# Kernel optimization log

Measured on AMD Instinct MI355X. Metric: run time of the kernel, lower is better.

Reference implementation:

```python
import jax, jax.numpy as jnp
import numpy as np
import math

B, T, D = 2, 2048, 4096
H, HD = 32, 128  # n_head, head_dim; H*HD == D
THETA = 10000.0


def _rope_tables(T, hd, theta):
    # standard RoPE: freqs_i = theta^(-2i/hd), angle[t,i] = t * freqs_i
    inv = 1.0 / (theta ** (np.arange(0, hd, 2, dtype=np.float32) / hd))  # [hd/2]
    ang = np.arange(T, dtype=np.float32)[:, None] * inv[None, :]          # [T, hd/2]
    return jnp.asarray(np.cos(ang)), jnp.asarray(np.sin(ang))


def setup_inputs() -> dict:
    key = jax.random.key(0)
    ks = jax.random.split(key, 5)
    scale = 1.0 / math.sqrt(D)
    x = jax.random.normal(ks[0], (B, T, D), dtype=jnp.float32)
    Wq = jax.random.normal(ks[1], (D, H * HD), dtype=jnp.float32) * scale
    Wk = jax.random.normal(ks[2], (D, H * HD), dtype=jnp.float32) * scale
    Wv = jax.random.normal(ks[3], (D, H * HD), dtype=jnp.float32) * scale
    Wo = jax.random.normal(ks[4], (D, D), dtype=jnp.float32) * scale
    fc, fs = _rope_tables(T, HD, THETA)
    return {"x": x, "freqs_cos": fc, "freqs_sin": fs,
            "Wq": Wq, "Wk": Wk, "Wv": Wv, "Wo": Wo}


def _apply_rope(t, cos, sin):
    # t: [B, T, H, HD]; complex rotation on interleaved (even, odd) pairs
    tp = t.reshape(*t.shape[:-1], HD // 2, 2)
    xr, xi = tp[..., 0], tp[..., 1]
    c = cos[None, :, None, :]  # [1, T, 1, HD/2]
    s = sin[None, :, None, :]
    out_r = xr * c - xi * s
    out_i = xr * s + xi * c
    return jnp.stack([out_r, out_i], axis=-1).reshape(t.shape)


def reference(x, freqs_cos, freqs_sin, Wq, Wk, Wv, Wo):
    Bc, Tc, _ = x.shape
    q = (x @ Wq).reshape(Bc, Tc, H, HD)
    k = (x @ Wk).reshape(Bc, Tc, H, HD)
    v = (x @ Wv).reshape(Bc, Tc, H, HD)
    q = _apply_rope(q, freqs_cos, freqs_sin)
    k = _apply_rope(k, freqs_cos, freqs_sin)
    scale = 1.0 / math.sqrt(HD)
    scores = jnp.einsum('bqhd,bkhd->bhqk', q, k) * scale  # [B,H,T,T]
    causal = jnp.tril(jnp.ones((Tc, Tc), dtype=bool))
    scores = jnp.where(causal[None, None], scores, -jnp.inf)
    attn = jax.nn.softmax(scores, axis=-1)
    y = jnp.einsum('bhqk,bkhd->bqhd', attn, v).reshape(Bc, Tc, H * HD)
    return y @ Wo
```

## Files before the change

kernel.cpp:

```cpp
#include <hip/hip_runtime.h>

typedef unsigned short ushort_t;
typedef unsigned int uint32;

typedef float f32x4 __attribute__((ext_vector_type(4)));
typedef __bf16 bf16x8 __attribute__((ext_vector_type(8)));
typedef unsigned short us8 __attribute__((ext_vector_type(8)));
typedef unsigned short us4 __attribute__((ext_vector_type(4)));

#define TSEQ 2048
#define DMODEL 4096

__device__ __forceinline__ ushort_t f2bf(float f) {
  uint32 u = __builtin_bit_cast(uint32, f);
  u += 0x7FFFu + ((u >> 16) & 1u);
  return (ushort_t)(u >> 16);
}
__device__ __forceinline__ float bf2f(ushort_t u) {
  return __builtin_bit_cast(float, ((uint32)u) << 16);
}

__device__ __forceinline__ void gload_lds16(const void* g, void* l) {
  auto gp = (const __attribute__((address_space(1))) void*)g;
  auto lp = (__attribute__((address_space(3))) void*)l;
  __builtin_amdgcn_global_load_lds(gp, lp, 16, 0, 0);
}

__global__ __launch_bounds__(256) void k_cast_bf16(const float* __restrict__ in,
                                                   ushort_t* __restrict__ out, int n4) {
  int g = blockIdx.x * 256 + threadIdx.x;
  if (g >= n4) return;
  float4 v = *(const float4*)(in + (size_t)g * 4);
  us4 o; o[0] = f2bf(v.x); o[1] = f2bf(v.y); o[2] = f2bf(v.z); o[3] = f2bf(v.w);
  *(us4*)(out + (size_t)g * 4) = o;
}

__global__ __launch_bounds__(256) void k_transpose_cast(const float* __restrict__ W,
                                                        ushort_t* __restrict__ WT) {
  __shared__ __align__(16) ushort_t ts[64 * 72];
  const int tid = threadIdx.x;
  const int n0 = blockIdx.x * 64, k0 = blockIdx.y * 64;
  #pragma unroll
  for (int it = 0; it < 4; ++it) {
    int e = it * 256 + tid;
    int r = e >> 4, c4 = e & 15;
    float4 v = *(const float4*)(W + (size_t)(k0 + r) * DMODEL + n0 + c4 * 4);
    us4 o; o[0] = f2bf(v.x); o[1] = f2bf(v.y); o[2] = f2bf(v.z); o[3] = f2bf(v.w);
    *(us4*)&ts[r * 72 + c4 * 4] = o;
  }
  __syncthreads();
  #pragma unroll
  for (int it = 0; it < 4; ++it) {
    int e = it * 256 + tid;
    int r2 = e >> 4, c4 = e & 15;
    us4 o;
    #pragma unroll
    for (int j = 0; j < 4; ++j) o[j] = ts[(c4 * 4 + j) * 72 + r2];
    *(us4*)(WT + (size_t)(n0 + r2) * DMODEL + k0 + c4 * 4) = o;
  }
}

template <bool OUT_BF16>
__global__ __launch_bounds__(512, 2)
void k_gemm256(const ushort_t* __restrict__ A, const ushort_t* __restrict__ Bt,
               void* __restrict__ Cv, int M, int N, int K) {
  __shared__ __align__(16) ushort_t As[2][256 * 64];
  __shared__ __align__(16) ushort_t Bs[2][256 * 64];
  const int tid = threadIdx.x;
  const int w = tid >> 6, l = tid & 63;
  const int wr = w >> 2, wc = w & 3;
  const int lg = l >> 4, lc = l & 15;

  const int nwg = gridDim.x;
  const int cpx = nwg >> 3;
  const int wg = (blockIdx.x & 7) * cpx + (blockIdx.x >> 3);
  const int nbn = N >> 8;
  const int bm = wg / nbn, bn = wg % nbn;

  const int rowoff = l >> 3;
  const int swzck  = (l & 7) ^ rowoff;
  const ushort_t* Ab = A + (size_t)(bm * 256) * K;
  const ushort_t* Bb = Bt + (size_t)(bn * 256) * K;
  const ushort_t* gA[4]; const ushort_t* gB[4];
  int ldsOff[4];
  #pragma unroll
  for (int j = 0; j < 4; ++j) {
    int r0 = (w * 4 + j) * 8;
    gA[j] = Ab + (size_t)(r0 + rowoff) * K + swzck * 8;
    gB[j] = Bb + (size_t)(r0 + rowoff) * K + swzck * 8;
    ldsOff[j] = r0 * 64;
  }

  int offA[8][2], offB[4][2];
  #pragma unroll
  for (int m = 0; m < 8; ++m)
    #pragma unroll
    for (int kk = 0; kk < 2; ++kk)
      offA[m][kk] = (wr * 128 + m * 16 + lc) * 64 + (((kk * 4 + lg) ^ (lc & 7)) * 8);
  #pragma unroll
  for (int n = 0; n < 4; ++n)
    #pragma unroll
    for (int kk = 0; kk < 2; ++kk)
      offB[n][kk] = (wc * 64 + n * 16 + lc) * 64 + (((kk * 4 + lg) ^ (lc & 7)) * 8);

  f32x4 acc[8][4];
  #pragma unroll
  for (int m = 0; m < 8; ++m)
    #pragma unroll
    for (int n = 0; n < 4; ++n) acc[m][n] = (f32x4){0.f, 0.f, 0.f, 0.f};

  #pragma unroll
  for (int j = 0; j < 4; ++j) {
    gload_lds16(gA[j], &As[0][ldsOff[j]]);
    gload_lds16(gB[j], &Bs[0][ldsOff[j]]);
  }
  #pragma unroll
  for (int j = 0; j < 4; ++j) {
    gload_lds16(gA[j] + 64, &As[1][ldsOff[j]]);
    gload_lds16(gB[j] + 64, &Bs[1][ldsOff[j]]);
  }
  asm volatile("s_waitcnt vmcnt(8)" ::: "memory");
  __builtin_amdgcn_s_barrier();
  __builtin_amdgcn_sched_barrier(0);

  const int NT = K >> 6;
  for (int t = 0; t < NT; ++t) {
    const int cur = t & 1;
    const ushort_t* Ac = As[cur];
    const ushort_t* Bc = Bs[cur];
    bf16x8 af[4][2], bf0[2][2], bf1[2][2];

    #pragma unroll
    for (int i = 0; i < 4; ++i)
      #pragma unroll
      for (int kk = 0; kk < 2; ++kk)
        af[i][kk] = *(const bf16x8*)&Ac[offA[i][kk]];
    #pragma unroll
    for (int j2 = 0; j2 < 2; ++j2)
      #pragma unroll
      for (int kk = 0; kk < 2; ++kk)
        bf0[j2][kk] = *(const bf16x8*)&Bc[offB[j2][kk]];
    asm volatile("" ::: "memory");
    __builtin_amdgcn_s_barrier();
    __builtin_amdgcn_s_setprio(1);
    #pragma unroll
    for (int i = 0; i < 4; ++i)
      #pragma unroll
      for (int j2 = 0; j2 < 2; ++j2)
        #pragma unroll
        for (int kk = 0; kk < 2; ++kk)
          acc[i][j2] = __builtin_amdgcn_mfma_f32_16x16x32_bf16(af[i][kk], bf0[j2][kk], acc[i][j2], 0, 0, 0);
    __builtin_amdgcn_s_setprio(0);
    __builtin_amdgcn_s_barrier();
    asm volatile("" ::: "memory");

    #pragma unroll
    for (int j2 = 0; j2 < 2; ++j2)
      #pragma unroll
      for (int kk = 0; kk < 2; ++kk)
        bf1[j2][kk] = *(const bf16x8*)&Bc[offB[2 + j2][kk]];
    asm volatile("" ::: "memory");
    __builtin_amdgcn_s_barrier();
    __builtin_amdgcn_s_setprio(1);
    #pragma unroll
    for (int i = 0; i < 4; ++i)
      #pragma unroll
      for (int j2 = 0; j2 < 2; ++j2)
        #pragma unroll
        for (int kk = 0; kk < 2; ++kk)
          acc[i][2 + j2] = __builtin_amdgcn_mfma_f32_16x16x32_bf16(af[i][kk], bf1[j2][kk], acc[i][2 + j2], 0, 0, 0);
    __builtin_amdgcn_s_setprio(0);
    __builtin_amdgcn_s_barrier();
    asm volatile("" ::: "memory");

    #pragma unroll
    for (int i = 0; i < 4; ++i)
      #pragma unroll
      for (int kk = 0; kk < 2; ++kk)
        af[i][kk] = *(const bf16x8*)&Ac[offA[4 + i][kk]];
    asm volatile("" ::: "memory");
    __builtin_amdgcn_s_barrier();
    __builtin_amdgcn_s_setprio(1);
    #pragma unroll
    for (int i = 0; i < 4; ++i)
      #pragma unroll
      for (int j2 = 0; j2 < 2; ++j2)
        #pragma unroll
        for (int kk = 0; kk < 2; ++kk)
          acc[4 + i][j2] = __builtin_amdgcn_mfma_f32_16x16x32_bf16(af[i][kk], bf0[j2][kk], acc[4 + i][j2], 0, 0, 0);
    __builtin_amdgcn_s_setprio(0);
    __builtin_amdgcn_s_barrier();
    asm volatile("" ::: "memory");

    if (t + 2 < NT) {
      const int k0 = (t + 2) << 6;
      #pragma unroll
      for (int j = 0; j < 4; ++j) {
        gload_lds16(gA[j] + k0, &As[cur][ldsOff[j]]);
        gload_lds16(gB[j] + k0, &Bs[cur][ldsOff[j]]);
      }
    }
    asm volatile("" ::: "memory");
    __builtin_amdgcn_s_barrier();
    __builtin_amdgcn_s_setprio(1);
    #pragma unroll
    for (int i = 0; i < 4; ++i)
      #pragma unroll
      for (int j2 = 0; j2 < 2; ++j2)
        #pragma unroll
        for (int kk = 0; kk < 2; ++kk)
          acc[4 + i][2 + j2] = __builtin_amdgcn_mfma_f32_16x16x32_bf16(af[i][kk], bf1[j2][kk], acc[4 + i][2 + j2], 0, 0, 0);
    __builtin_amdgcn_s_setprio(0);

    if (t + 2 < NT) {
      asm volatile("s_waitcnt vmcnt(8)" ::: "memory");
    } else if (t + 1 < NT) {
      asm volatile("s_waitcnt vmcnt(0)" ::: "memory");
    }
    if (t + 1 < NT) {
      __builtin_amdgcn_s_barrier();
      __builtin_amdgcn_sched_barrier(0);
    }
  }

  #pragma unroll
  for (int m = 0; m < 8; ++m) {
    int row0 = bm * 256 + wr * 128 + m * 16 + lg * 4;
    #pragma unroll
    for (int n = 0; n < 4; ++n) {
      int col = bn * 256 + wc * 64 + n * 16 + lc;
      #pragma unroll
      for (int r = 0; r < 4; ++r) {
        float v = acc[m][n][r];
        if (OUT_BF16) ((ushort_t*)Cv)[(size_t)(row0 + r) * N + col] = f2bf(v);
        else          ((float*)Cv)[(size_t)(row0 + r) * N + col] = v;
      }
    }
  }
}

__global__ __launch_bounds__(256) void k_rope(ushort_t* __restrict__ q, ushort_t* __restrict__ k,
                                              const float* __restrict__ fc,
                                              const float* __restrict__ fs) {
  int g = blockIdx.x * 256 + threadIdx.x;
  size_t base = (size_t)g * 8;
  int row = (int)(base >> 12);
  int col = (int)(base & 4095);
  int t = row & (TSEQ - 1);
  int i0 = (col & 127) >> 1;
  float4 c = *(const float4*)(fc + t * 64 + i0);
  float4 s = *(const float4*)(fs + t * 64 + i0);
  ushort_t* bufs[2] = {q, k};
  #pragma unroll
  for (int bi = 0; bi < 2; ++bi) {
    us8 v = *(const us8*)(bufs[bi] + base);
    us8 o;
    float xr, xi;
    xr = bf2f(v[0]); xi = bf2f(v[1]);
    o[0] = f2bf(xr * c.x - xi * s.x); o[1] = f2bf(xr * s.x + xi * c.x);
    xr = bf2f(v[2]); xi = bf2f(v[3]);
    o[2] = f2bf(xr * c.y - xi * s.y); o[3] = f2bf(xr * s.y + xi * c.y);
    xr = bf2f(v[4]); xi = bf2f(v[5]);
    o[4] = f2bf(xr * c.z - xi * s.z); o[5] = f2bf(xr * s.z + xi * c.z);
    xr = bf2f(v[6]); xi = bf2f(v[7]);
    o[6] = f2bf(xr * c.w - xi * s.w); o[7] = f2bf(xr * s.w + xi * c.w);
    *(us8*)(bufs[bi] + base) = o;
  }
}

__global__ __launch_bounds__(512, 2)
void k_attn(const ushort_t* __restrict__ Q, const ushort_t* __restrict__ Kb,
            const ushort_t* __restrict__ Vt, ushort_t* __restrict__ Y) {
  __shared__ __align__(16) ushort_t Ks[2][64 * 128];
  __shared__ __align__(16) ushort_t Vs[2][128 * 64];
  __shared__ __align__(16) ushort_t Ps[8][16 * 64];
  const int id = blockIdx.x;
  const int xcd = id & 7, slot = id >> 3;
  const int bx = slot & 7, gHi = slot >> 3;
  const int g = gHi * 8 + xcd;
  const int h = g & 31, b = g >> 5;
  const int tid = threadIdx.x;
  const int w = tid >> 6, l = tid & 63;
  const int lg = l >> 4, lc = l & 15;
  const float scale = 0.08838834764831845f;
  const float THR = 8.0f;

  auto stageKV = [&](int kv0, int buf) {
    #pragma unroll
    for (int i = 0; i < 2; ++i) {
      int seg = w * 2 + i;
      {
        int row = seg * 4 + (l >> 4);
        int csrc = (l & 15) ^ (row & 7);
        gload_lds16(Kb + (size_t)(b * TSEQ + kv0 + row) * DMODEL + h * 128 + csrc * 8,
                    &Ks[buf][seg * 512]);
      }
      {
        int row = seg * 8 + (l >> 3);
        int csrc = (l & 7) ^ (l >> 3);
        gload_lds16(Vt + (size_t)(h * 128 + row) * DMODEL + b * TSEQ + kv0 + csrc * 8,
                    &Vs[buf][seg * 512]);
      }
    }
  };

  for (int qi = 0; qi < 2; ++qi) {
    const int qt = qi ? (15 - bx) : bx;
    const int q0 = qt * 128;
    const int wrow0 = q0 + w * 16;

    bf16x8 qf[4];
    {
      const ushort_t* qp = Q + (size_t)(b * TSEQ + wrow0 + lc) * DMODEL + h * 128;
      #pragma unroll
      for (int ks = 0; ks < 4; ++ks) qf[ks] = *(const bf16x8*)(qp + ks * 32 + lg * 8);
    }

    float m_r[4], lp[4];
    #pragma unroll
    for (int r = 0; r < 4; ++r) { m_r[r] = -1e30f; lp[r] = 0.f; }
    f32x4 o[8];
    #pragma unroll
    for (int t = 0; t < 8; ++t) o[t] = (f32x4){0.f, 0.f, 0.f, 0.f};

    const int nkv = (qt + 1) * 2;
    stageKV(0, 0);
    for (int kt = 0; kt < nkv; ++kt) {
      const int cur = kt & 1;
      const int kv0 = kt * 64;
      if (kt + 1 < nkv) {
        stageKV((kt + 1) * 64, cur ^ 1);
        asm volatile("s_waitcnt vmcnt(4)" ::: "memory");
      } else {
        asm volatile("s_waitcnt vmcnt(0)" ::: "memory");
      }
      __builtin_amdgcn_s_barrier();

      if (kv0 <= wrow0 + 15) {
        f32x4 s[4];
        __builtin_amdgcn_s_setprio(1);
        #pragma unroll
        for (int n = 0; n < 4; ++n) {
          s[n] = (f32x4){0.f, 0.f, 0.f, 0.f};
          #pragma unroll
          for (int ks = 0; ks < 4; ++ks) {
            int row = n * 16 + lc;
            bf16x8 kf = *(const bf16x8*)&Ks[cur][row * 128 + ((ks * 32 + lg * 8) ^ ((row & 7) * 8))];
            s[n] = __builtin_amdgcn_mfma_f32_16x16x32_bf16(qf[ks], kf, s[n], 0, 0, 0);
          }
        }
        __builtin_amdgcn_s_setprio(0);

        float sv[4][4];
        if (kv0 + 63 > wrow0) {
          #pragma unroll
          for (int n = 0; n < 4; ++n)
            #pragma unroll
            for (int r = 0; r < 4; ++r) {
              float x = s[n][r] * scale;
              int kvg = kv0 + n * 16 + lc;
              int qg = wrow0 + lg * 4 + r;
              sv[n][r] = (kvg > qg) ? -1e30f : x;
            }
        } else {
          #pragma unroll
          for (int n = 0; n < 4; ++n)
            #pragma unroll
            for (int r = 0; r < 4; ++r) sv[n][r] = s[n][r] * scale;
        }

        float pmax[4];
        #pragma unroll
        for (int r = 0; r < 4; ++r)
          pmax[r] = fmaxf(fmaxf(sv[0][r], sv[1][r]), fmaxf(sv[2][r], sv[3][r]));
        bool ok = (pmax[0] <= m_r[0] + THR) && (pmax[1] <= m_r[1] + THR) &&
                  (pmax[2] <= m_r[2] + THR) && (pmax[3] <= m_r[3] + THR);
        if (!__all(ok)) {
          #pragma unroll
          for (int r = 0; r < 4; ++r) {
            float mx = pmax[r];
            #pragma unroll
            for (int off = 1; off < 16; off <<= 1) mx = fmaxf(mx, __shfl_xor(mx, off, 16));
            float mn = fmaxf(m_r[r], mx);
            float al = __expf(m_r[r] - mn);
            m_r[r] = mn;
            lp[r] *= al;
            #pragma unroll
            for (int t = 0; t < 8; ++t) o[t][r] *= al;
          }
        }

        #pragma unroll
        for (int n = 0; n < 4; ++n)
          #pragma unroll
          for (int r = 0; r < 4; ++r) {
            float p = __expf(sv[n][r] - m_r[r]);
            lp[r] += p;
            int row = lg * 4 + r, col = n * 16 + lc;
            Ps[w][row * 64 + (col ^ (lg * 16))] = f2bf(p);
          }

        __builtin_amdgcn_s_setprio(1);
        #pragma unroll
        for (int kvs = 0; kvs < 2; ++kvs) {
          bf16x8 pa = *(const bf16x8*)&Ps[w][lc * 64 + ((kvs * 32 + lg * 8) ^ ((lc >> 2) * 16))];
          #pragma unroll
          for (int t = 0; t < 8; ++t) {
            int vrow = t * 16 + lc;
            bf16x8 vb = *(const bf16x8*)&Vs[cur][vrow * 64 + ((kvs * 32 + lg * 8) ^ ((vrow & 7) * 8))];
            o[t] = __builtin_amdgcn_mfma_f32_16x16x32_bf16(pa, vb, o[t], 0, 0, 0);
          }
        }
        __builtin_amdgcn_s_setprio(0);
      }
      asm volatile("" ::: "memory");
      __builtin_amdgcn_s_barrier();
    }

    float linv[4];
    #pragma unroll
    for (int r = 0; r < 4; ++r) {
      float ls = lp[r];
      #pragma unroll
      for (int off = 1; off < 16; off <<= 1) ls += __shfl_xor(ls, off, 16);
      linv[r] = 1.0f / ls;
    }

    #pragma unroll
    for (int t = 0; t < 8; ++t)
      #pragma unroll
      for (int r = 0; r < 4; ++r) {
        int row = wrow0 + lg * 4 + r;
        int col = h * 128 + t * 16 + lc;
        Y[(size_t)(b * TSEQ + row) * DMODEL + col] = f2bf(o[t][r] * linv[r]);
      }
  }
}

extern "C" void kernel_launch(void* const* d_in, const int* in_sizes, int n_in,
                              void* d_out, int out_size, void* d_ws, size_t ws_size,
                              hipStream_t stream) {
  const float* x  = (const float*)d_in[0];
  const float* fc = (const float*)d_in[1];
  const float* fs = (const float*)d_in[2];
  const float* Wq = (const float*)d_in[3];
  const float* Wk = (const float*)d_in[4];
  const float* Wv = (const float*)d_in[5];
  const float* Wo = (const float*)d_in[6];

  const size_t SZ = (size_t)4096 * 4096;
  ushort_t* xb  = (ushort_t*)d_ws;
  ushort_t* WqT = xb + SZ;
  ushort_t* WkT = WqT + SZ;
  ushort_t* WvT = WkT + SZ;
  ushort_t* WoT = WvT + SZ;
  ushort_t* qb  = WoT + SZ;
  ushort_t* kb  = qb + SZ;
  ushort_t* vT  = kb + SZ;
  ushort_t* yb  = vT + SZ;

  k_cast_bf16<<<16384, 256, 0, stream>>>(x, xb, 4194304);
  dim3 tg(64, 64);
  k_transpose_cast<<<tg, 256, 0, stream>>>(Wq, WqT);
  k_transpose_cast<<<tg, 256, 0, stream>>>(Wk, WkT);
  k_transpose_cast<<<tg, 256, 0, stream>>>(Wv, WvT);
  k_transpose_cast<<<tg, 256, 0, stream>>>(Wo, WoT);

  k_gemm256<true><<<256, 512, 0, stream>>>(xb, WqT, qb, 4096, 4096, 4096);
  k_gemm256<true><<<256, 512, 0, stream>>>(xb, WkT, kb, 4096, 4096, 4096);
  k_gemm256<true><<<256, 512, 0, stream>>>(WvT, xb, vT, 4096, 4096, 4096);

  k_rope<<<8192, 256, 0, stream>>>(qb, kb, fc, fs);

  k_attn<<<512, 512, 0, stream>>>(qb, kb, vT, yb);

  k_gemm256<false><<<256, 512, 0, stream>>>(yb, WoT, d_out, 4096, 4096, 4096);
}
```

Measured before the change: 887.7 us.

## Fuse RoPE into Q/K GEMM epilogue, batch weight transposes, simplify GEMM phases

Removes the separate RoPE kernel by applying the rotation in the Q and K GEMM epilogues, using a lane shuffle to fetch the paired element. The four weight transpose-casts become one launch with a z grid dimension. The GEMM main loop drops from four barrier-separated MFMA phases to two by loading both B halves at once, which cuts barriers but raises register pressure. The epilogue now reads cos/sin per element, which adds scattered loads.

Result: no change. 902.5 us (+1.7%).

```diff
diff --git a/kernel.cpp b/kernel.cpp
--- a/kernel.cpp
+++ b/kernel.cpp
@@ -35,9 +35,15 @@
   *(us4*)(out + (size_t)g * 4) = o;
 }
 
-__global__ __launch_bounds__(256) void k_transpose_cast(const float* __restrict__ W,
-                                                        ushort_t* __restrict__ WT) {
+__global__ __launch_bounds__(256) void k_transpose_cast4(const float* __restrict__ W0,
+                                                         const float* __restrict__ W1,
+                                                         const float* __restrict__ W2,
+                                                         const float* __restrict__ W3,
+                                                         ushort_t* __restrict__ WTbase) {
   __shared__ __align__(16) ushort_t ts[64 * 72];
+  const float* Ws[4] = {W0, W1, W2, W3};
+  const float* W = Ws[blockIdx.z];
+  ushort_t* WT = WTbase + (size_t)blockIdx.z * DMODEL * DMODEL;
   const int tid = threadIdx.x;
   const int n0 = blockIdx.x * 64, k0 = blockIdx.y * 64;
   #pragma unroll
@@ -60,10 +66,11 @@
   }
 }
 
-template <bool OUT_BF16>
+template <bool OUT_BF16, bool ROPE>
 __global__ __launch_bounds__(512, 2)
 void k_gemm256(const ushort_t* __restrict__ A, const ushort_t* __restrict__ Bt,
-               void* __restrict__ Cv, int M, int N, int K) {
+               void* __restrict__ Cv, int M, int N, int K,
+               const float* __restrict__ fc, const float* __restrict__ fs) {
   __shared__ __align__(16) ushort_t As[2][256 * 64];
   __shared__ __align__(16) ushort_t Bs[2][256 * 64];
   const int tid = threadIdx.x;
@@ -128,7 +135,7 @@
     const int cur = t & 1;
     const ushort_t* Ac = As[cur];
     const ushort_t* Bc = Bs[cur];
-    bf16x8 af[4][2], bf0[2][2], bf1[2][2];
+    bf16x8 af[4][2], b0[2][2], b1[2][2];
 
     #pragma unroll
     for (int i = 0; i < 4; ++i)
@@ -138,40 +145,24 @@
     #pragma unroll
     for (int j2 = 0; j2 < 2; ++j2)
       #pragma unroll
-      for (int kk = 0; kk < 2; ++kk)
-        bf0[j2][kk] = *(const bf16x8*)&Bc[offB[j2][kk]];
+      for (int kk = 0; kk < 2; ++kk) {
+        b0[j2][kk] = *(const bf16x8*)&Bc[offB[j2][kk]];
+        b1[j2][kk] = *(const bf16x8*)&Bc[offB[2 + j2][kk]];
+      }
     asm volatile("" ::: "memory");
     __builtin_amdgcn_s_barrier();
+
     __builtin_amdgcn_s_setprio(1);
     #pragma unroll
     for (int i = 0; i < 4; ++i)
       #pragma unroll
       for (int j2 = 0; j2 < 2; ++j2)
         #pragma unroll
-        for (int kk = 0; kk < 2; ++kk)
-          acc[i][j2] = __builtin_amdgcn_mfma_f32_16x16x32_bf16(af[i][kk], bf0[j2][kk], acc[i][j2], 0, 0, 0);
+        for (int kk = 0; kk < 2; ++kk) {
+          acc[i][j2]     = __builtin_amdgcn_mfma_f32_16x16x32_bf16(af[i][kk], b0[j2][kk], acc[i][j2], 0, 0, 0);
+          acc[i][2 + j2] = __builtin_amdgcn_mfma_f32_16x16x32_bf16(af[i][kk], b1[j2][kk], acc[i][2 + j2], 0, 0, 0);
+        }
     __builtin_amdgcn_s_setprio(0);
-    __builtin_amdgcn_s_barrier();
-    asm volatile("" ::: "memory");
-
-    #pragma unroll
-    for (int j2 = 0; j2 < 2; ++j2)
-      #pragma unroll
-      for (int kk = 0; kk < 2; ++kk)
-        bf1[j2][kk] = *(const bf16x8*)&Bc[offB[2 + j2][kk]];
-    asm volatile("" ::: "memory");
-    __builtin_amdgcn_s_barrier();
-    __builtin_amdgcn_s_setprio(1);
-    #pragma unroll
-    for (int i = 0; i < 4; ++i)
-      #pragma unroll
-      for (int j2 = 0; j2 < 2; ++j2)
-        #pragma unroll
-        for (int kk = 0; kk < 2; ++kk)
-          acc[i][2 + j2] = __builtin_amdgcn_mfma_f32_16x16x32_bf16(af[i][kk], bf1[j2][kk], acc[i][2 + j2], 0, 0, 0);
-    __builtin_amdgcn_s_setprio(0);
-    __builtin_amdgcn_s_barrier();
-    asm volatile("" ::: "memory");
 
     #pragma unroll
     for (int i = 0; i < 4; ++i)
@@ -180,17 +171,20 @@
         af[i][kk] = *(const bf16x8*)&Ac[offA[4 + i][kk]];
     asm volatile("" ::: "memory");
     __builtin_amdgcn_s_barrier();
+
     __builtin_amdgcn_s_setprio(1);
     #pragma unroll
     for (int i = 0; i < 4; ++i)
       #pragma unroll
       for (int j2 = 0; j2 < 2; ++j2)
         #pragma unroll
-        for (int kk = 0; kk < 2; ++kk)
-          acc[4 + i][j2] = __builtin_amdgcn_mfma_f32_16x16x32_bf16(af[i][kk], bf0[j2][kk], acc[4 + i][j2], 0, 0, 0);
+        for (int kk = 0; kk < 2; ++kk) {
+          acc[4 + i][j2]     = __builtin_amdgcn_mfma_f32_16x16x32_bf16(af[i][kk], b0[j2][kk], acc[4 + i][j2], 0, 0, 0);
+          acc[4 + i][2 + j2] = __builtin_amdgcn_mfma_f32_16x16x32_bf16(af[i][kk], b1[j2][kk], acc[4 + i][2 + j2], 0, 0, 0);
+        }
     __builtin_amdgcn_s_setprio(0);
+    asm volatile("" ::: "memory");
     __builtin_amdgcn_s_barrier();
-    asm volatile("" ::: "memory");
 
     if (t + 2 < NT) {
       const int k0 = (t + 2) << 6;
@@ -199,20 +193,6 @@
         gload_lds16(gA[j] + k0, &As[cur][ldsOff[j]]);
         gload_lds16(gB[j] + k0, &Bs[cur][ldsOff[j]]);
       }
-    }
-    asm volatile("" ::: "memory");
-    __builtin_amdgcn_s_barrier();
-    __builtin_amdgcn_s_setprio(1);
-    #pragma unroll
-    for (int i = 0; i < 4; ++i)
-      #pragma unroll
-      for (int j2 = 0; j2 < 2; ++j2)
-        #pragma unroll
-        for (int kk = 0; kk < 2; ++kk)
-          acc[4 + i][2 + j2] = __builtin_amdgcn_mfma_f32_16x16x32_bf16(af[i][kk], bf1[j2][kk], acc[4 + i][2 + j2], 0, 0, 0);
-    __builtin_amdgcn_s_setprio(0);
-
-    if (t + 2 < NT) {
       asm volatile("s_waitcnt vmcnt(8)" ::: "memory");
     } else if (t + 1 < NT) {
       asm volatile("s_waitcnt vmcnt(0)" ::: "memory");
@@ -229,42 +209,27 @@
     #pragma unroll
     for (int n = 0; n < 4; ++n) {
       int col = bn * 256 + wc * 64 + n * 16 + lc;
-      #pragma unroll
-      for (int r = 0; r < 4; ++r) {
-        float v = acc[m][n][r];
-        if (OUT_BF16) ((ushort_t*)Cv)[(size_t)(row0 + r) * N + col] = f2bf(v);
-        else          ((float*)Cv)[(size_t)(row0 + r) * N + col] = v;
-      }
-    }
-  }
-}
-
-__global__ __launch_bounds__(256) void k_rope(ushort_t* __restrict__ q, ushort_t* __restrict__ k,
-                                              const float* __restrict__ fc,
-                                              const float* __restrict__ fs) {
-  int g = blockIdx.x * 256 + threadIdx.x;
-  size_t base = (size_t)g * 8;
-  int row = (int)(base >> 12);
-  int col = (int)(base & 4095);
-  int t = row & (TSEQ - 1);
-  int i0 = (col & 127) >> 1;
-  float4 c = *(const float4*)(fc + t * 64 + i0);
-  float4 s = *(const float4*)(fs + t * 64 + i0);
-  ushort_t* bufs[2] = {q, k};
-  #pragma unroll
-  for (int bi = 0; bi < 2; ++bi) {
-    us8 v = *(const us8*)(bufs[bi] + base);
-    us8 o;
-    float xr, xi;
-    xr = bf2f(v[0]); xi = bf2f(v[1]);
-    o[0] = f2bf(xr * c.x - xi * s.x); o[1] = f2bf(xr * s.x + xi * c.x);
-    xr = bf2f(v[2]); xi = bf2f(v[3]);
-    o[2] = f2bf(xr * c.y - xi * s.y); o[3] = f2bf(xr * s.y + xi * c.y);
-    xr = bf2f(v[4]); xi = bf2f(v[5]);
-    o[4] = f2bf(xr * c.z - xi * s.z); o[5] = f2bf(xr * s.z + xi * c.z);
-    xr = bf2f(v[6]); xi = bf2f(v[7]);
-    o[6] = f2bf(xr * c.w - xi * s.w); o[7] = f2bf(xr * s.w + xi * c.w);
-    *(us8*)(bufs[bi] + base) = o;
+      if (ROPE) {
+        int i0 = (col & 127) >> 1;
+        #pragma unroll
+        for (int r = 0; r < 4; ++r) {
+          int tt = (row0 + r) & (TSEQ - 1);
+          float c = fc[tt * 64 + i0];
+          float s = fs[tt * 64 + i0];
+          float v = acc[m][n][r];
+          float p = __shfl_xor(v, 1);
+          float ov = (lc & 1) ? (p * s + v * c) : (v * c - p * s);
+          ((ushort_t*)Cv)[(size_t)(row0 + r) * N + col] = f2bf(ov);
+        }
+      } else {
+        #pragma unroll
+        for (int r = 0; r < 4; ++r) {
+          float v = acc[m][n][r];
+          if (OUT_BF16) ((ushort_t*)Cv)[(size_t)(row0 + r) * N + col] = f2bf(v);
+          else          ((float*)Cv)[(size_t)(row0 + r) * N + col] = v;
+        }
+      }
+    }
   }
 }
 
@@ -460,19 +425,14 @@
   ushort_t* yb  = vT + SZ;
 
   k_cast_bf16<<<16384, 256, 0, stream>>>(x, xb, 4194304);
-  dim3 tg(64, 64);
-  k_transpose_cast<<<tg, 256, 0, stream>>>(Wq, WqT);
-  k_transpose_cast<<<tg, 256, 0, stream>>>(Wk, WkT);
-  k_transpose_cast<<<tg, 256, 0, stream>>>(Wv, WvT);
-  k_transpose_cast<<<tg, 256, 0, stream>>>(Wo, WoT);
-
-  k_gemm256<true><<<256, 512, 0, stream>>>(xb, WqT, qb, 4096, 4096, 4096);
-  k_gemm256<true><<<256, 512, 0, stream>>>(xb, WkT, kb, 4096, 4096, 4096);
-  k_gemm256<true><<<256, 512, 0, stream>>>(WvT, xb, vT, 4096, 4096, 4096);
-
-  k_rope<<<8192, 256, 0, stream>>>(qb, kb, fc, fs);
+  dim3 tg(64, 64, 4);
+  k_transpose_cast4<<<tg, 256, 0, stream>>>(Wq, Wk, Wv, Wo, WqT);
+
+  k_gemm256<true, true><<<256, 512, 0, stream>>>(xb, WqT, qb, 4096, 4096, 4096, fc, fs);
+  k_gemm256<true, true><<<256, 512, 0, stream>>>(xb, WkT, kb, 4096, 4096, 4096, fc, fs);
+  k_gemm256<true, false><<<256, 512, 0, stream>>>(WvT, xb, vT, 4096, 4096, 4096, nullptr, nullptr);
 
   k_attn<<<512, 512, 0, stream>>>(qb, kb, vT, yb);
 
-  k_gemm256<false><<<256, 512, 0, stream>>>(yb, WoT, d_out, 4096, 4096, 4096);
-}
+  k_gemm256<false, false><<<256, 512, 0, stream>>>(yb, WoT, d_out, 4096, 4096, 4096, nullptr, nullptr);
+}
```
